# Performance work log

Measured on AMD Instinct MI355X. Metric: run time of the kernel, lower is better.

## Reference

```python
import jax, jax.numpy as jnp
import numpy as np

B, L = 4096, 200
USER_COUNT, ITEM_COUNT, CATE_COUNT = 100000, 100000, 1000
USER_DIM, ITEM_DIM, CATE_DIM = 128, 64, 64
BN_EPS = 1e-5


def setup_inputs() -> dict:
    key = jax.random.key(0)
    ks = jax.random.split(key, 16)
    # ragged history: valid prefix of `length` items (ids >= 1), zero-padded tail
    length = jax.random.randint(ks[3], (B,), 1, L + 1)
    hist_raw = jax.random.randint(ks[2], (B, L), 1, ITEM_COUNT)
    history = jnp.where(jnp.arange(L)[None, :] < length[:, None], hist_raw, 0)
    inp = {
        "user": jax.random.randint(ks[0], (B,), 0, USER_COUNT),
        "item": jax.random.randint(ks[1], (B,), 0, ITEM_COUNT),
        "history": history,
        "length": length,
        "cate_list": jax.random.randint(ks[4], (ITEM_COUNT,), 0, CATE_COUNT),
        "user_emb_W": jax.random.normal(ks[5], (USER_COUNT, USER_DIM), jnp.float32) * 0.05,
        "item_emb_W": jax.random.normal(ks[6], (ITEM_COUNT, ITEM_DIM), jnp.float32) * 0.05,
        "cate_emb_W": jax.random.normal(ks[7], (CATE_COUNT, CATE_DIM), jnp.float32) * 0.05,
        "bn_gamma": 1.0 + 0.1 * jax.random.normal(ks[8], (384,), jnp.float32),
        "bn_beta": 0.1 * jax.random.normal(ks[9], (384,), jnp.float32),
        "W1": jax.random.normal(ks[10], (200, 384), jnp.float32) * (1.0 / np.sqrt(384)),
        "b1": jnp.zeros((200,), jnp.float32),
        "a1": jnp.full((), 0.25, jnp.float32),
        "W2": jax.random.normal(ks[11], (80, 200), jnp.float32) * (1.0 / np.sqrt(200)),
        "b2": jnp.zeros((80,), jnp.float32),
        "a2": jnp.full((), 0.25, jnp.float32),
        "W3": jax.random.normal(ks[12], (2, 80), jnp.float32) * (1.0 / np.sqrt(80)),
        "b3": jnp.zeros((2,), jnp.float32),
    }
    return inp


def _prelu(x, a):
    return jnp.where(x >= 0, x, a * x)


def reference(user, item, history, length, cate_list,
              user_emb_W, item_emb_W, cate_emb_W, bn_gamma, bn_beta,
              W1, b1, a1, W2, b2, a2, W3, b3):
    u = user_emb_W[user]                                              # [B,128]
    it = jnp.concatenate([item_emb_W[item], cate_emb_W[cate_list[item]]], -1)  # [B,128]

    # Faithful replication of get_emb's loop semantics:
    # row b uses the prefix of `history[b]` up to (and incl.) the position
    # just before the first zero; a row whose first entry is 0 halts the
    # outer loop, zeroing that row and all following rows.
    nz = history != 0                                                 # [B,L]
    prefix = jnp.concatenate(
        [jnp.ones((history.shape[0], 1), bool),
         jnp.cumprod(nz[:, 1:].astype(jnp.int32), axis=1).astype(bool)], axis=1)
    row_active = jnp.cumprod(nz[:, 0].astype(jnp.int32)).astype(bool)  # outer break
    mask = prefix & row_active[:, None]                               # [B,L]

    he = jnp.concatenate([item_emb_W[history], cate_emb_W[cate_list[history]]], -1)  # [B,L,128]
    cnt = jnp.maximum(mask.sum(-1), 1).astype(he.dtype)               # [B]
    pooled = (he * mask[..., None].astype(he.dtype)).sum(1) / cnt[:, None]  # [B,128]

    x = jnp.concatenate([u, it, pooled], -1)                          # [B,384]
    # BatchNorm1d in training mode (batch stats, biased variance)
    mean = x.mean(0)
    var = x.var(0)
    x = (x - mean) * jax.lax.rsqrt(var + BN_EPS) * bn_gamma + bn_beta
    x = _prelu(x @ W1.T + b1, a1)
    x = _prelu(x @ W2.T + b2, a2)
    x = x @ W3.T + b3
    return jax.nn.softmax(x, axis=1)
```

## Files before the change

### kernel.cpp

```cpp
#include <hip/hip_runtime.h>
#include <hip/hip_bf16.h>

#define B_SZ 4096
#define L_SZ 200

typedef __bf16 bf16x8 __attribute__((ext_vector_type(8)));
typedef float  f32x4  __attribute__((ext_vector_type(4)));

static __device__ inline unsigned short bfbits(float f) {
    return __builtin_bit_cast(unsigned short, (__bf16)f);
}
static __device__ inline float bf2f(unsigned short u) {
    return __builtin_bit_cast(float, (unsigned int)u << 16);
}

__global__ __launch_bounds__(1024) void k_prep(const int* __restrict__ history,
                                               int* __restrict__ first_bad,
                                               float* __restrict__ acc) {
    const int tid = threadIdx.x;
    if (tid < 768) acc[tid] = 0.f;
    int m = B_SZ;
    for (int b = tid; b < B_SZ; b += 1024)
        if (history[(size_t)b * L_SZ] == 0) m = min(m, b);
    __shared__ int red[1024];
    red[tid] = m;
    __syncthreads();
    for (int s = 512; s > 0; s >>= 1) {
        if (tid < s) red[tid] = min(red[tid], red[tid + s]);
        __syncthreads();
    }
    if (tid == 0) first_bad[0] = red[0];
}

__global__ __launch_bounds__(64) void k_wfrag(const float* __restrict__ W1,
                                              const float* __restrict__ W2,
                                              ushort* __restrict__ W1f,
                                              ushort* __restrict__ W2f) {
    const int bid = blockIdx.x, lane = threadIdx.x;
    const int nr = lane & 15, quad = lane >> 4;
    ushort v[8];
    if (bid < 156) {
        const int oT = bid / 12, kS = bid % 12;
        const int o = oT * 16 + nr;
        #pragma unroll
        for (int j = 0; j < 8; ++j) {
            int k = kS * 32 + quad * 8 + j;
            v[j] = (o < 200) ? bfbits(W1[(size_t)o * 384 + k]) : (ushort)0;
        }
        ushort* dst = W1f + ((size_t)bid * 64 + lane) * 8;
        *(ushort4*)(dst)     = make_ushort4(v[0], v[1], v[2], v[3]);
        *(ushort4*)(dst + 4) = make_ushort4(v[4], v[5], v[6], v[7]);
    } else {
        const int idx = bid - 156;
        const int oT = idx / 7, kS = idx % 7;
        const int o = oT * 16 + nr;
        #pragma unroll
        for (int j = 0; j < 8; ++j) {
            int k = kS * 32 + quad * 8 + j;
            v[j] = (k < 200) ? bfbits(W2[(size_t)o * 200 + k]) : (ushort)0;
        }
        ushort* dst = W2f + ((size_t)idx * 64 + lane) * 8;
        *(ushort4*)(dst)     = make_ushort4(v[0], v[1], v[2], v[3]);
        *(ushort4*)(dst + 4) = make_ushort4(v[4], v[5], v[6], v[7]);
    }
}

__global__ __launch_bounds__(256) void k_pool(
    const int* __restrict__ user, const int* __restrict__ item,
    const int* __restrict__ history, const int* __restrict__ cate_list,
    const float* __restrict__ user_W, const float* __restrict__ item_W,
    const float* __restrict__ cate_W, const int* __restrict__ first_bad,
    ushort* __restrict__ xb)
{
    const int b = blockIdx.x;
    const int tid = threadIdx.x;
    __shared__ int sh_item[L_SZ];
    __shared__ int sh_cid[L_SZ];
    __shared__ int s_fz;
    __shared__ __align__(16) float red[8][128];
    if (tid == 0) s_fz = L_SZ;
    __syncthreads();
    if (tid < L_SZ) {
        int h = history[(size_t)b * L_SZ + tid];
        sh_item[tid] = h;
        if (tid >= 1 && h == 0) atomicMin(&s_fz, tid);
        sh_cid[tid] = cate_list[h];
    }
    __syncthreads();
    const bool active = (b < first_bad[0]);
    const int valid = active ? s_fz : 0;
    const float inv_cnt = 1.0f / (float)max(valid, 1);

    const int group = tid >> 5, lane = tid & 31;
    const int sub = lane >> 4, q = lane & 15;
    const float* tab = (sub == 0) ? item_W : cate_W;
    const int*   ids = (sub == 0) ? sh_item : sh_cid;
    float4 acc = make_float4(0.f, 0.f, 0.f, 0.f);
    int l = group;
    for (; l + 8 < valid; l += 16) {
        int id0 = ids[l], id1 = ids[l + 8];
        float4 v0 = ((const float4*)(tab + (size_t)id0 * 64))[q];
        float4 v1 = ((const float4*)(tab + (size_t)id1 * 64))[q];
        acc.x += v0.x + v1.x; acc.y += v0.y + v1.y;
        acc.z += v0.z + v1.z; acc.w += v0.w + v1.w;
    }
    if (l < valid) {
        int id = ids[l];
        float4 v = ((const float4*)(tab + (size_t)id * 64))[q];
        acc.x += v.x; acc.y += v.y; acc.z += v.z; acc.w += v.w;
    }
    *((float4*)&red[group][lane * 4]) = acc;
    __syncthreads();

    ushort* xrow = xb + (size_t)b * 384;
    if (tid < 128) {
        float s = 0.f;
        #pragma unroll
        for (int g = 0; g < 8; ++g) s += red[g][tid];
        xrow[256 + tid] = bfbits(s * inv_cnt);
        xrow[tid] = bfbits(user_W[(size_t)user[b] * 128 + tid]);
    } else if (tid < 192) {
        int f = tid - 128;
        xrow[128 + f] = bfbits(item_W[(size_t)item[b] * 64 + f]);
    } else {
        int f = tid - 192;
        xrow[192 + f] = bfbits(cate_W[(size_t)cate_list[item[b]] * 64 + f]);
    }
}

__global__ __launch_bounds__(384) void k_bnstats(const ushort* __restrict__ xb,
                                                 float* __restrict__ acc) {
    const int f = threadIdx.x;
    const int r0 = blockIdx.x * 32;
    float s = 0.f, s2 = 0.f;
    for (int r = r0; r < r0 + 32; ++r) {
        float v = bf2f(xb[(size_t)r * 384 + f]);
        s += v; s2 += v * v;
    }
    atomicAdd(&acc[f], s);
    atomicAdd(&acc[384 + f], s2);
}

__global__ __launch_bounds__(256) void k_l1(
    const ushort* __restrict__ xb, const float* __restrict__ accv,
    const float* __restrict__ gamma, const float* __restrict__ beta,
    const ushort* __restrict__ W1f, const float* __restrict__ b1,
    const float* __restrict__ a1p, ushort* __restrict__ h1b)
{
    __shared__ float As[384], Cs[384];
    const int tid = threadIdx.x;
    for (int f = tid; f < 384; f += 256) {
        const float inv_b = 1.0f / (float)B_SZ;
        float mean = accv[f] * inv_b;
        float var  = accv[384 + f] * inv_b - mean * mean;
        float a = gamma[f] * rsqrtf(var + 1e-5f);
        As[f] = a;
        Cs[f] = beta[f] - mean * a;
    }
    __syncthreads();

    const int lane = tid & 63, wv = tid >> 6;
    const int nr = lane & 15, quad = lane >> 4;
    const int wid = blockIdx.x * 4 + wv;
    const int mT = wid / 13, oT = wid - mT * 13;
    const int o = oT * 16 + nr;
    const float a1 = a1p[0];

    float bias = (o < 200) ? b1[o] : 0.f;
    f32x4 acc = {bias, bias, bias, bias};
    const ushort* xrow = xb + (size_t)(mT * 16 + nr) * 384;

    for (int kS = 0; kS < 12; ++kS) {
        const int kc = kS * 32 + quad * 8;
        bf16x8 a8 = *(const bf16x8*)(xrow + kc);
        float4 A0 = *(const float4*)&As[kc],     A1 = *(const float4*)&As[kc + 4];
        float4 C0 = *(const float4*)&Cs[kc],     C1 = *(const float4*)&Cs[kc + 4];
        bf16x8 w;
        w[0] = (__bf16)((float)a8[0] * A0.x + C0.x);
        w[1] = (__bf16)((float)a8[1] * A0.y + C0.y);
        w[2] = (__bf16)((float)a8[2] * A0.z + C0.z);
        w[3] = (__bf16)((float)a8[3] * A0.w + C0.w);
        w[4] = (__bf16)((float)a8[4] * A1.x + C1.x);
        w[5] = (__bf16)((float)a8[5] * A1.y + C1.y);
        w[6] = (__bf16)((float)a8[6] * A1.z + C1.z);
        w[7] = (__bf16)((float)a8[7] * A1.w + C1.w);
        bf16x8 bfr = *(const bf16x8*)(W1f + (((size_t)oT * 12 + kS) * 64 + lane) * 8);
        acc = __builtin_amdgcn_mfma_f32_16x16x32_bf16(w, bfr, acc, 0, 0, 0);
    }

    #pragma unroll
    for (int r = 0; r < 4; ++r) {
        int row = mT * 16 + quad * 4 + r;
        float s = acc[r];
        s = (s >= 0.f) ? s : a1 * s;
        h1b[(size_t)row * 224 + o] = bfbits(s);
        if (oT == 12) h1b[(size_t)row * 224 + o + 16] = 0;
    }
}

__global__ __launch_bounds__(256) void k_l23(
    const ushort* __restrict__ h1b, const ushort* __restrict__ W2f,
    const float* __restrict__ b2, const float* __restrict__ a2p,
    const float* __restrict__ W3, const float* __restrict__ b3,
    float* __restrict__ out)
{
    const int tid = threadIdx.x;
    const int lane = tid & 63, wv = tid >> 6;
    const int nr = lane & 15, quad = lane >> 4;
    const int mT = blockIdx.x * 4 + wv;
    const float a2 = a2p[0];

    f32x4 acc[5];
    #pragma unroll
    for (int i = 0; i < 5; ++i) {
        float bb = b2[i * 16 + nr];
        acc[i] = (f32x4){bb, bb, bb, bb};
    }
    const ushort* hrow = h1b + (size_t)(mT * 16 + nr) * 224;
    for (int kS = 0; kS < 7; ++kS) {
        bf16x8 a8 = *(const bf16x8*)(hrow + kS * 32 + quad * 8);
        #pragma unroll
        for (int i = 0; i < 5; ++i) {
            bf16x8 bfr = *(const bf16x8*)(W2f + (((size_t)i * 7 + kS) * 64 + lane) * 8);
            acc[i] = __builtin_amdgcn_mfma_f32_16x16x32_bf16(a8, bfr, acc[i], 0, 0, 0);
        }
    }

    float w0[5], w1[5];
    #pragma unroll
    for (int i = 0; i < 5; ++i) {
        w0[i] = W3[i * 16 + nr];
        w1[i] = W3[80 + i * 16 + nr];
    }
    f32x4 p0 = {0.f, 0.f, 0.f, 0.f}, p1 = {0.f, 0.f, 0.f, 0.f};
    #pragma unroll
    for (int i = 0; i < 5; ++i) {
        #pragma unroll
        for (int r = 0; r < 4; ++r) {
            float s = acc[i][r];
            s = (s >= 0.f) ? s : a2 * s;
            p0[r] += s * w0[i];
            p1[r] += s * w1[i];
        }
    }
    #pragma unroll
    for (int m = 1; m < 16; m <<= 1) {
        #pragma unroll
        for (int r = 0; r < 4; ++r) {
            p0[r] += __shfl_xor(p0[r], m, 64);
            p1[r] += __shfl_xor(p1[r], m, 64);
        }
    }
    if (nr == 0) {
        float B0 = b3[0], B1 = b3[1];
        #pragma unroll
        for (int r = 0; r < 4; ++r) {
            float l0 = p0[r] + B0, l1 = p1[r] + B1;
            float mx = fmaxf(l0, l1);
            float e0 = expf(l0 - mx), e1 = expf(l1 - mx);
            float inv = 1.0f / (e0 + e1);
            int row = mT * 16 + quad * 4 + r;
            *(float2*)(out + (size_t)row * 2) = make_float2(e0 * inv, e1 * inv);
        }
    }
}

extern "C" void kernel_launch(void* const* d_in, const int* in_sizes, int n_in,
                              void* d_out, int out_size, void* d_ws, size_t ws_size,
                              hipStream_t stream) {
    const int*   user      = (const int*)  d_in[0];
    const int*   item      = (const int*)  d_in[1];
    const int*   history   = (const int*)  d_in[2];
    const int*   cate_list = (const int*)  d_in[4];
    const float* user_W    = (const float*)d_in[5];
    const float* item_W    = (const float*)d_in[6];
    const float* cate_W    = (const float*)d_in[7];
    const float* gamma     = (const float*)d_in[8];
    const float* beta      = (const float*)d_in[9];
    const float* W1        = (const float*)d_in[10];
    const float* b1        = (const float*)d_in[11];
    const float* a1        = (const float*)d_in[12];
    const float* W2        = (const float*)d_in[13];
    const float* b2        = (const float*)d_in[14];
    const float* a2        = (const float*)d_in[15];
    const float* W3        = (const float*)d_in[16];
    const float* b3        = (const float*)d_in[17];
    float* out = (float*)d_out;

    char* ws = (char*)d_ws;
    int*    first_bad = (int*)   ws;
    float*  acc       = (float*)(ws + 64);
    ushort* xb        = (ushort*)(ws + 3200);
    ushort* h1b       = (ushort*)(ws + 3148928);
    ushort* W1f       = (ushort*)(ws + 4983936);
    ushort* W2f       = (ushort*)(ws + 5143680);

    hipLaunchKernelGGL(k_prep,    dim3(1),    dim3(1024), 0, stream, history, first_bad, acc);
    hipLaunchKernelGGL(k_wfrag,   dim3(191),  dim3(64),   0, stream, W1, W2, W1f, W2f);
    hipLaunchKernelGGL(k_pool,    dim3(B_SZ), dim3(256),  0, stream,
                       user, item, history, cate_list, user_W, item_W, cate_W,
                       first_bad, xb);
    hipLaunchKernelGGL(k_bnstats, dim3(128),  dim3(384),  0, stream, xb, acc);
    hipLaunchKernelGGL(k_l1,      dim3(832),  dim3(256),  0, stream,
                       xb, acc, gamma, beta, W1f, b1, a1, h1b);
    hipLaunchKernelGGL(k_l23,     dim3(64),   dim3(256),  0, stream,
                       h1b, W2f, b2, a2, W3, b3, out);
}
```

Baseline: 182.1 us.

## Convert embedding tables to bf16 per call and gather bf16 rows in pooling

A new pre-kernel converts the full item and category embedding tables to bf16 on every call. The same kernel merges the weight-fragment packing and the first-bad-row scan, so fewer kernels are launched. Pooling now gathers 16-byte bf16 rows with 16 parallel row groups instead of fp32 float4 rows. The outer-loop row masking moves out of pooling into bnstats and layer 1, which lets pooling start without waiting on the first-bad value. The trade-off is a 25.6 MB read and 12.8 MB write of the whole item table per call, against gathers that only touch a subset of rows.

```diff
diff --git a/kernel.cpp b/kernel.cpp
--- a/kernel.cpp
+++ b/kernel.cpp
@@ -14,54 +14,74 @@
     return __builtin_bit_cast(float, (unsigned int)u << 16);
 }
 
-__global__ __launch_bounds__(1024) void k_prep(const int* __restrict__ history,
-                                               int* __restrict__ first_bad,
-                                               float* __restrict__ acc) {
-    const int tid = threadIdx.x;
-    if (tid < 768) acc[tid] = 0.f;
-    int m = B_SZ;
-    for (int b = tid; b < B_SZ; b += 1024)
-        if (history[(size_t)b * L_SZ] == 0) m = min(m, b);
-    __shared__ int red[1024];
-    red[tid] = m;
-    __syncthreads();
-    for (int s = 512; s > 0; s >>= 1) {
-        if (tid < s) red[tid] = min(red[tid], red[tid + s]);
+#define NB_ICVT 6250
+#define NB_CCVT 63
+#define NB_WFR  48
+
+__global__ __launch_bounds__(256) void k_pre(
+    const float* __restrict__ item_W, const float* __restrict__ cate_W,
+    const float* __restrict__ W1, const float* __restrict__ W2,
+    const int* __restrict__ history,
+    ushort* __restrict__ item_bf, ushort* __restrict__ cate_bf,
+    ushort* __restrict__ W1f, ushort* __restrict__ W2f,
+    int* __restrict__ first_bad, float* __restrict__ acc)
+{
+    const int bid = blockIdx.x, tid = threadIdx.x;
+    if (bid < NB_ICVT) {
+        int idx = bid * 256 + tid;
+        float4 v = ((const float4*)item_W)[idx];
+        ((ushort4*)item_bf)[idx] =
+            make_ushort4(bfbits(v.x), bfbits(v.y), bfbits(v.z), bfbits(v.w));
+    } else if (bid < NB_ICVT + NB_CCVT) {
+        int idx = (bid - NB_ICVT) * 256 + tid;
+        if (idx < 16000) {
+            float4 v = ((const float4*)cate_W)[idx];
+            ((ushort4*)cate_bf)[idx] =
+                make_ushort4(bfbits(v.x), bfbits(v.y), bfbits(v.z), bfbits(v.w));
+        }
+    } else if (bid < NB_ICVT + NB_CCVT + NB_WFR) {
+        const int chunk = (bid - NB_ICVT - NB_CCVT) * 4 + (tid >> 6);
+        const int lane = tid & 63, nr = lane & 15, quad = lane >> 4;
+        if (chunk < 191) {
+            ushort v[8];
+            if (chunk < 156) {
+                const int oT = chunk / 12, kS = chunk % 12;
+                const int o = oT * 16 + nr;
+                #pragma unroll
+                for (int j = 0; j < 8; ++j) {
+                    int k = kS * 32 + quad * 8 + j;
+                    v[j] = (o < 200) ? bfbits(W1[(size_t)o * 384 + k]) : (ushort)0;
+                }
+                ushort* dst = W1f + ((size_t)chunk * 64 + lane) * 8;
+                *(ushort4*)(dst)     = make_ushort4(v[0], v[1], v[2], v[3]);
+                *(ushort4*)(dst + 4) = make_ushort4(v[4], v[5], v[6], v[7]);
+            } else {
+                const int idx = chunk - 156;
+                const int oT = idx / 7, kS = idx % 7;
+                const int o = oT * 16 + nr;
+                #pragma unroll
+                for (int j = 0; j < 8; ++j) {
+                    int k = kS * 32 + quad * 8 + j;
+                    v[j] = (k < 200) ? bfbits(W2[(size_t)o * 200 + k]) : (ushort)0;
+                }
+                ushort* dst = W2f + ((size_t)idx * 64 + lane) * 8;
+                *(ushort4*)(dst)     = make_ushort4(v[0], v[1], v[2], v[3]);
+                *(ushort4*)(dst + 4) = make_ushort4(v[4], v[5], v[6], v[7]);
+            }
+        }
+    } else {
+        acc[tid] = 0.f; acc[256 + tid] = 0.f; acc[512 + tid] = 0.f;
+        int m = B_SZ;
+        for (int b = tid; b < B_SZ; b += 256)
+            if (history[(size_t)b * L_SZ] == 0) m = min(m, b);
+        __shared__ int red[256];
+        red[tid] = m;
         __syncthreads();
-    }
-    if (tid == 0) first_bad[0] = red[0];
-}
-
-__global__ __launch_bounds__(64) void k_wfrag(const float* __restrict__ W1,
-                                              const float* __restrict__ W2,
-                                              ushort* __restrict__ W1f,
-                                              ushort* __restrict__ W2f) {
-    const int bid = blockIdx.x, lane = threadIdx.x;
-    const int nr = lane & 15, quad = lane >> 4;
-    ushort v[8];
-    if (bid < 156) {
-        const int oT = bid / 12, kS = bid % 12;
-        const int o = oT * 16 + nr;
-        #pragma unroll
-        for (int j = 0; j < 8; ++j) {
-            int k = kS * 32 + quad * 8 + j;
-            v[j] = (o < 200) ? bfbits(W1[(size_t)o * 384 + k]) : (ushort)0;
-        }
-        ushort* dst = W1f + ((size_t)bid * 64 + lane) * 8;
-        *(ushort4*)(dst)     = make_ushort4(v[0], v[1], v[2], v[3]);
-        *(ushort4*)(dst + 4) = make_ushort4(v[4], v[5], v[6], v[7]);
-    } else {
-        const int idx = bid - 156;
-        const int oT = idx / 7, kS = idx % 7;
-        const int o = oT * 16 + nr;
-        #pragma unroll
-        for (int j = 0; j < 8; ++j) {
-            int k = kS * 32 + quad * 8 + j;
-            v[j] = (k < 200) ? bfbits(W2[(size_t)o * 200 + k]) : (ushort)0;
-        }
-        ushort* dst = W2f + ((size_t)idx * 64 + lane) * 8;
-        *(ushort4*)(dst)     = make_ushort4(v[0], v[1], v[2], v[3]);
-        *(ushort4*)(dst + 4) = make_ushort4(v[4], v[5], v[6], v[7]);
+        for (int s = 128; s > 0; s >>= 1) {
+            if (tid < s) red[tid] = min(red[tid], red[tid + s]);
+            __syncthreads();
+        }
+        if (tid == 0) first_bad[0] = red[0];
     }
 }
 
@@ -69,7 +89,8 @@
     const int* __restrict__ user, const int* __restrict__ item,
     const int* __restrict__ history, const int* __restrict__ cate_list,
     const float* __restrict__ user_W, const float* __restrict__ item_W,
-    const float* __restrict__ cate_W, const int* __restrict__ first_bad,
+    const float* __restrict__ cate_W,
+    const ushort* __restrict__ item_bf, const ushort* __restrict__ cate_bf,
     ushort* __restrict__ xb)
 {
     const int b = blockIdx.x;
@@ -77,7 +98,7 @@
     __shared__ int sh_item[L_SZ];
     __shared__ int sh_cid[L_SZ];
     __shared__ int s_fz;
-    __shared__ __align__(16) float red[8][128];
+    __shared__ __align__(16) float red[16][128];
     if (tid == 0) s_fz = L_SZ;
     __syncthreads();
     if (tid < L_SZ) {
@@ -87,36 +108,37 @@
         sh_cid[tid] = cate_list[h];
     }
     __syncthreads();
-    const bool active = (b < first_bad[0]);
-    const int valid = active ? s_fz : 0;
+    const int valid = s_fz;
     const float inv_cnt = 1.0f / (float)max(valid, 1);
 
-    const int group = tid >> 5, lane = tid & 31;
-    const int sub = lane >> 4, q = lane & 15;
-    const float* tab = (sub == 0) ? item_W : cate_W;
-    const int*   ids = (sub == 0) ? sh_item : sh_cid;
-    float4 acc = make_float4(0.f, 0.f, 0.f, 0.f);
-    int l = group;
-    for (; l + 8 < valid; l += 16) {
-        int id0 = ids[l], id1 = ids[l + 8];
-        float4 v0 = ((const float4*)(tab + (size_t)id0 * 64))[q];
-        float4 v1 = ((const float4*)(tab + (size_t)id1 * 64))[q];
-        acc.x += v0.x + v1.x; acc.y += v0.y + v1.y;
-        acc.z += v0.z + v1.z; acc.w += v0.w + v1.w;
+    const int p = tid >> 4, sub = (tid >> 3) & 1, q = tid & 7;
+    const ushort* tab = sub ? cate_bf : item_bf;
+    const int*    ids = sub ? sh_cid : sh_item;
+    float a0 = 0.f, a1_ = 0.f, a2_ = 0.f, a3 = 0.f, a4 = 0.f, a5 = 0.f, a6 = 0.f, a7 = 0.f;
+    int l = p;
+    for (; l + 16 < valid; l += 32) {
+        bf16x8 v0 = *(const bf16x8*)(tab + (size_t)ids[l] * 64 + q * 8);
+        bf16x8 v1 = *(const bf16x8*)(tab + (size_t)ids[l + 16] * 64 + q * 8);
+        a0 += (float)v0[0] + (float)v1[0]; a1_ += (float)v0[1] + (float)v1[1];
+        a2_ += (float)v0[2] + (float)v1[2]; a3 += (float)v0[3] + (float)v1[3];
+        a4 += (float)v0[4] + (float)v1[4]; a5 += (float)v0[5] + (float)v1[5];
+        a6 += (float)v0[6] + (float)v1[6]; a7 += (float)v0[7] + (float)v1[7];
     }
     if (l < valid) {
-        int id = ids[l];
-        float4 v = ((const float4*)(tab + (size_t)id * 64))[q];
-        acc.x += v.x; acc.y += v.y; acc.z += v.z; acc.w += v.w;
-    }
-    *((float4*)&red[group][lane * 4]) = acc;
+        bf16x8 v0 = *(const bf16x8*)(tab + (size_t)ids[l] * 64 + q * 8);
+        a0 += (float)v0[0]; a1_ += (float)v0[1]; a2_ += (float)v0[2]; a3 += (float)v0[3];
+        a4 += (float)v0[4]; a5 += (float)v0[5]; a6 += (float)v0[6]; a7 += (float)v0[7];
+    }
+    float* rp = &red[p][sub * 64 + q * 8];
+    *(float4*)(rp)     = make_float4(a0, a1_, a2_, a3);
+    *(float4*)(rp + 4) = make_float4(a4, a5, a6, a7);
     __syncthreads();
 
     ushort* xrow = xb + (size_t)b * 384;
     if (tid < 128) {
         float s = 0.f;
         #pragma unroll
-        for (int g = 0; g < 8; ++g) s += red[g][tid];
+        for (int g = 0; g < 16; ++g) s += red[g][tid];
         xrow[256 + tid] = bfbits(s * inv_cnt);
         xrow[tid] = bfbits(user_W[(size_t)user[b] * 128 + tid]);
     } else if (tid < 192) {
@@ -129,12 +151,16 @@
 }
 
 __global__ __launch_bounds__(384) void k_bnstats(const ushort* __restrict__ xb,
+                                                 const int* __restrict__ first_bad,
                                                  float* __restrict__ acc) {
     const int f = threadIdx.x;
-    const int r0 = blockIdx.x * 32;
+    const int r0 = blockIdx.x * 64;
+    const int fb = first_bad[0];
+    const bool pooled = (f >= 256);
     float s = 0.f, s2 = 0.f;
-    for (int r = r0; r < r0 + 32; ++r) {
+    for (int r = r0; r < r0 + 64; ++r) {
         float v = bf2f(xb[(size_t)r * 384 + f]);
+        if (pooled && r >= fb) v = 0.f;
         s += v; s2 += v * v;
     }
     atomicAdd(&acc[f], s);
@@ -145,7 +171,8 @@
     const ushort* __restrict__ xb, const float* __restrict__ accv,
     const float* __restrict__ gamma, const float* __restrict__ beta,
     const ushort* __restrict__ W1f, const float* __restrict__ b1,
-    const float* __restrict__ a1p, ushort* __restrict__ h1b)
+    const float* __restrict__ a1p, const int* __restrict__ first_bad,
+    ushort* __restrict__ h1b)
 {
     __shared__ float As[384], Cs[384];
     const int tid = threadIdx.x;
@@ -165,16 +192,41 @@
     const int mT = wid / 13, oT = wid - mT * 13;
     const int o = oT * 16 + nr;
     const float a1 = a1p[0];
+    const int fb = first_bad[0];
+    const bool badrow = (mT * 16 + nr) >= fb;
 
     float bias = (o < 200) ? b1[o] : 0.f;
     f32x4 acc = {bias, bias, bias, bias};
     const ushort* xrow = xb + (size_t)(mT * 16 + nr) * 384;
 
-    for (int kS = 0; kS < 12; ++kS) {
+    #pragma unroll 2
+    for (int kS = 0; kS < 8; ++kS) {
         const int kc = kS * 32 + quad * 8;
         bf16x8 a8 = *(const bf16x8*)(xrow + kc);
-        float4 A0 = *(const float4*)&As[kc],     A1 = *(const float4*)&As[kc + 4];
-        float4 C0 = *(const float4*)&Cs[kc],     C1 = *(const float4*)&Cs[kc + 4];
+        float4 A0 = *(const float4*)&As[kc], A1 = *(const float4*)&As[kc + 4];
+        float4 C0 = *(const float4*)&Cs[kc], C1 = *(const float4*)&Cs[kc + 4];
+        bf16x8 w;
+        w[0] = (__bf16)((float)a8[0] * A0.x + C0.x);
+        w[1] = (__bf16)((float)a8[1] * A0.y + C0.y);
+        w[2] = (__bf16)((float)a8[2] * A0.z + C0.z);
+        w[3] = (__bf16)((float)a8[3] * A0.w + C0.w);
+        w[4] = (__bf16)((float)a8[4] * A1.x + C1.x);
+        w[5] = (__bf16)((float)a8[5] * A1.y + C1.y);
+        w[6] = (__bf16)((float)a8[6] * A1.z + C1.z);
+        w[7] = (__bf16)((float)a8[7] * A1.w + C1.w);
+        bf16x8 bfr = *(const bf16x8*)(W1f + (((size_t)oT * 12 + kS) * 64 + lane) * 8);
+        acc = __builtin_amdgcn_mfma_f32_16x16x32_bf16(w, bfr, acc, 0, 0, 0);
+    }
+    #pragma unroll 2
+    for (int kS = 8; kS < 12; ++kS) {
+        const int kc = kS * 32 + quad * 8;
+        bf16x8 a8 = *(const bf16x8*)(xrow + kc);
+        if (badrow) {
+            #pragma unroll
+            for (int j = 0; j < 8; ++j) a8[j] = (__bf16)0.f;
+        }
+        float4 A0 = *(const float4*)&As[kc], A1 = *(const float4*)&As[kc + 4];
+        float4 C0 = *(const float4*)&Cs[kc], C1 = *(const float4*)&Cs[kc + 4];
         bf16x8 w;
         w[0] = (__bf16)((float)a8[0] * A0.x + C0.x);
         w[1] = (__bf16)((float)a8[1] * A0.y + C0.y);
@@ -294,15 +346,18 @@
     ushort* h1b       = (ushort*)(ws + 3148928);
     ushort* W1f       = (ushort*)(ws + 4983936);
     ushort* W2f       = (ushort*)(ws + 5143680);
-
-    hipLaunchKernelGGL(k_prep,    dim3(1),    dim3(1024), 0, stream, history, first_bad, acc);
-    hipLaunchKernelGGL(k_wfrag,   dim3(191),  dim3(64),   0, stream, W1, W2, W1f, W2f);
-    hipLaunchKernelGGL(k_pool,    dim3(B_SZ), dim3(256),  0, stream,
+    ushort* item_bf   = (ushort*)(ws + 5179520);
+    ushort* cate_bf   = (ushort*)(ws + 17979520);
+
+    hipLaunchKernelGGL(k_pre,     dim3(NB_ICVT + NB_CCVT + NB_WFR + 1), dim3(256), 0, stream,
+                       item_W, cate_W, W1, W2, history,
+                       item_bf, cate_bf, W1f, W2f, first_bad, acc);
+    hipLaunchKernelGGL(k_pool,    dim3(B_SZ), dim3(256), 0, stream,
                        user, item, history, cate_list, user_W, item_W, cate_W,
-                       first_bad, xb);
-    hipLaunchKernelGGL(k_bnstats, dim3(128),  dim3(384),  0, stream, xb, acc);
-    hipLaunchKernelGGL(k_l1,      dim3(832),  dim3(256),  0, stream,
-                       xb, acc, gamma, beta, W1f, b1, a1, h1b);
-    hipLaunchKernelGGL(k_l23,     dim3(64),   dim3(256),  0, stream,
+                       item_bf, cate_bf, xb);
+    hipLaunchKernelGGL(k_bnstats, dim3(64),   dim3(384), 0, stream, xb, first_bad, acc);
+    hipLaunchKernelGGL(k_l1,      dim3(832),  dim3(256), 0, stream,
+                       xb, acc, gamma, beta, W1f, b1, a1, first_bad, h1b);
+    hipLaunchKernelGGL(k_l23,     dim3(64),   dim3(256), 0, stream,
                        h1b, W2f, b2, a2, W3, b3, out);
 }
```

Result: no change. 181.5 us (-0.3%).
